# Optimization experiments

Hardware: AMD Instinct MI355X
Metric: run time of the kernel (lower is better)

## Reference

```python
import jax, jax.numpy as jnp
import numpy as np

B, T, D = 4, 1024, 1024
H = 16
DH = D // H            # head dim (attention_dim/num_heads)
FF = 4096
EPS = 1e-6             # allennlp LayerNorm eps
NEG = jnp.finfo(jnp.float32).min


def _layer_norm(x, g, b):
    # allennlp LayerNorm: (x - mean) / (unbiased_std + eps) * gamma + beta
    mean = jnp.mean(x, axis=-1, keepdims=True)
    var = jnp.var(x, axis=-1, keepdims=True) * (x.shape[-1] / (x.shape[-1] - 1))
    return g * (x - mean) / (jnp.sqrt(var) + EPS) + b


def setup_inputs() -> dict:
    key = jax.random.key(0)
    ks = jax.random.split(key, 12)
    s = lambda fan_in: 1.0 / np.sqrt(fan_in)
    return {
        "src": jax.random.normal(ks[0], (B, T, D), jnp.float32),
        "src_mask": jnp.ones((B, T), jnp.int32),
        # weights stored [in, out]
        "q_w": jax.random.uniform(ks[1], (D, D), jnp.float32, -s(D), s(D)),
        "q_b": jnp.zeros((D,), jnp.float32),
        "kv_w": jax.random.uniform(ks[2], (D, 2 * D), jnp.float32, -s(D), s(D)),
        "kv_b": jnp.zeros((2 * D,), jnp.float32),
        "out_w": jax.random.uniform(ks[3], (D, D), jnp.float32, -s(D), s(D)),
        "out_b": jnp.zeros((D,), jnp.float32),
        "ffn_w1": jax.random.uniform(ks[4], (D, FF), jnp.float32, -s(D), s(D)),
        "ffn_b1": jnp.zeros((FF,), jnp.float32),
        "ffn_w2": jax.random.uniform(ks[5], (FF, D), jnp.float32, -s(FF), s(FF)),
        "ffn_b2": jnp.zeros((D,), jnp.float32),
        "norm1_g": jnp.ones((D,), jnp.float32),
        "norm1_b": jnp.zeros((D,), jnp.float32),
        "norm2_g": jnp.ones((D,), jnp.float32),
        "norm2_b": jnp.zeros((D,), jnp.float32),
    }


def reference(src, src_mask, q_w, q_b, kv_w, kv_b, out_w, out_b,
              ffn_w1, ffn_b1, ffn_w2, ffn_b2,
              norm1_g, norm1_b, norm2_g, norm2_b):
    b, t, d = src.shape
    scale = jnp.asarray(DH ** 0.5, src.dtype)

    q = (src @ q_w + q_b).reshape(b, t, H, DH)
    kv = src @ kv_w + kv_b                         # (b,t,2D): first half keys, second half values
    k = kv[..., :D].reshape(b, t, H, DH)
    v = kv[..., D:].reshape(b, t, H, DH)

    # scaled dot-product: queries divided by sqrt(head_dim) before bmm
    logits = jnp.einsum("bqhd,bkhd->bhqk", q / scale, k)
    # memory_efficient masked_softmax: masked key positions -> dtype min
    mask = src_mask[:, None, None, :].astype(bool)  # (b,1,1,t) over keys
    logits = jnp.where(mask, logits, NEG)
    attn = jax.nn.softmax(logits, axis=-1)          # dropout off (eval)

    ctx = jnp.einsum("bhqk,bkhd->bqhd", attn, v).reshape(b, t, D)
    attn_out = ctx @ out_w + out_b

    out1 = _layer_norm(src + attn_out, norm1_g, norm1_b)
    ffn = jax.nn.relu(out1 @ ffn_w1 + ffn_b1) @ ffn_w2 + ffn_b2
    out2 = _layer_norm(out1 + ffn, norm2_g, norm2_b)
    return out2
```

## Files before the change

kernel.cpp:

```cpp
#include <hip/hip_runtime.h>

#define DEV __device__ __forceinline__
#define SB0 __builtin_amdgcn_sched_barrier(0)

typedef unsigned short u16;
typedef __attribute__((ext_vector_type(4))) float f32x4;
typedef __attribute__((ext_vector_type(8))) short short8;

DEV u16 f2bf(float f) {
  union { float f; unsigned u; } c; c.f = f;
  unsigned u = c.u;
  unsigned r = (u + 0x7FFFu + ((u >> 16) & 1u)) >> 16;
  return (u16)r;
}
DEV float bf2f(u16 h) {
  union { unsigned u; float f; } c; c.u = ((unsigned)h) << 16;
  return c.f;
}
DEV unsigned cvtpk(float a, float b) {
  unsigned r;
  asm("v_cvt_pk_bf16_f32 %0, %1, %2" : "=v"(r) : "v"(a), "v"(b));
  return r;
}

DEV void gload16(const void* g, void* l) {
  __builtin_amdgcn_global_load_lds(
      (__attribute__((address_space(1))) void*)(g),
      (__attribute__((address_space(3))) void*)(l), 16, 0, 0);
}
DEV void vmc8() { asm volatile("s_waitcnt vmcnt(8)" ::: "memory"); SB0; }
DEV void vmc0() { asm volatile("s_waitcnt vmcnt(0)" ::: "memory"); SB0; }

__global__ __launch_bounds__(256) void prep_kernel(
    const float* __restrict__ src, const float* __restrict__ q_w,
    const float* __restrict__ kv_w, const float* __restrict__ out_w,
    const float* __restrict__ w1, const float* __restrict__ w2,
    u16* __restrict__ Xbf, u16* __restrict__ WqkvT, u16* __restrict__ WoT,
    u16* __restrict__ W1T, u16* __restrict__ W2T) {
  __shared__ float tile[32 * 33];
  int bb = blockIdx.x, tid = threadIdx.x;
  if (bb < 4096) {
    int i = bb * 256 + tid;
    float4 v = reinterpret_cast<const float4*>(src)[i];
    ushort4 o;
    o.x = f2bf(v.x); o.y = f2bf(v.y); o.z = f2bf(v.z); o.w = f2bf(v.w);
    reinterpret_cast<ushort4*>(Xbf)[i] = o;
    return;
  }
  const float* in; u16* outp; int ld_in, ld_out, bx, by;
  if (bb < 5120)       { int t = bb - 4096;  in = q_w;   outp = WqkvT; ld_in = 1024; ld_out = 1024; bx = t & 31;  by = t >> 5; }
  else if (bb < 7168)  { int t = bb - 5120;  in = kv_w;  outp = WqkvT + (size_t)1024 * 1024; ld_in = 2048; ld_out = 1024; bx = t & 63;  by = t >> 6; }
  else if (bb < 8192)  { int t = bb - 7168;  in = out_w; outp = WoT;   ld_in = 1024; ld_out = 1024; bx = t & 31;  by = t >> 5; }
  else if (bb < 12288) { int t = bb - 8192;  in = w1;    outp = W1T;   ld_in = 4096; ld_out = 1024; bx = t & 127; by = t >> 7; }
  else                 { int t = bb - 12288; in = w2;    outp = W2T;   ld_in = 1024; ld_out = 4096; bx = t & 31;  by = t >> 5; }
  int tx = tid & 31, ty = tid >> 5;
  int c0 = bx * 32, r0 = by * 32;
#pragma unroll
  for (int j = 0; j < 4; ++j)
    tile[(ty + j * 8) * 33 + tx] = in[(size_t)(r0 + ty + j * 8) * ld_in + c0 + tx];
  __syncthreads();
#pragma unroll
  for (int j = 0; j < 4; ++j)
    outp[(size_t)(c0 + ty + j * 8) * ld_out + r0 + tx] = f2bf(tile[tx * 33 + ty + j * 8]);
}

__global__ __launch_bounds__(256) void transpose_vtp_kernel(
    const u16* __restrict__ in, u16* __restrict__ out) {
  __shared__ float tile[32][33];
  int c0 = blockIdx.x * 32, r0 = blockIdx.y * 32;
  int tx = threadIdx.x, ty = threadIdx.y;
#pragma unroll
  for (int j = 0; j < 4; ++j)
    tile[ty + j * 8][tx] = bf2f(in[(size_t)(r0 + ty + j * 8) * 3072 + 2048 + c0 + tx]);
  __syncthreads();
  int k = r0 + tx;
  int base = k & ~63, kb = k & 63;
  int n = kb >> 4, w = kb & 15;
  int p = ((n >> 1) << 5) | ((w >> 2) << 3) | ((n & 1) << 2) | (w & 3);
#pragma unroll
  for (int j = 0; j < 4; ++j)
    out[(size_t)(c0 + ty + j * 8) * 4096 + base + p] = f2bf(tile[tx][ty + j * 8]);
}

template <int BM, int NWARP, typename OutT, bool RELU>
__global__ __launch_bounds__(NWARP * 64, 2) void gemm_ring_kernel(
    const u16* __restrict__ A, int lda,
    const u16* __restrict__ Bt, int ldb,
    const float* __restrict__ bias, const float* __restrict__ bias2, int split,
    OutT* __restrict__ C, int ldc, int K, float scale) {
  constexpr int MT = BM / 32;
  constexpr int PWR = BM / 2;
  constexpr int WN = NWARP / 2;
  constexpr int SLOT = 2 * BM * 32;
  __shared__ __align__(16) u16 ring[4][SLOT];

  const int tid = threadIdx.x;
  const int lane = tid & 63, wid = tid >> 6;
  const int wr = wid / WN, wc = wid % WN;
  const int lr = lane & 15, hi = lane >> 4;

  const int gx = gridDim.x;
  const int nwg = gx * gridDim.y;
  const int orig = blockIdx.y * gx + blockIdx.x;
  const int q = nwg >> 3, r8 = nwg & 7, xcd = orig & 7, oo = orig >> 3;
  const int lid = (xcd < r8 ? xcd * (q + 1) : r8 * (q + 1) + (xcd - r8) * q) + oo;
  const int rb = lid / gx, cb = lid % gx;

  const u16* Abase = A + (size_t)rb * BM * lda;
  const u16* Bbase = Bt + (size_t)cb * BM * ldb;

  auto stage = [&](int slot, int kt) {
#pragma unroll
    for (int j = 0; j < 2; ++j) {
      int ch = wid * 2 + j;
      int row = ch * 16 + (lane >> 2);
      int cs = (lane & 3) ^ ((row >> 1) & 3);
      gload16(Abase + (size_t)row * lda + kt * 32 + cs * 8, &ring[slot][ch * 512]);
      gload16(Bbase + (size_t)row * ldb + kt * 32 + cs * 8, &ring[slot][BM * 32 + ch * 512]);
    }
  };

  f32x4 acc[MT][4];
  const f32x4 zero = {0.f, 0.f, 0.f, 0.f};
#pragma unroll
  for (int m = 0; m < MT; ++m)
#pragma unroll
    for (int n = 0; n < 4; ++n) acc[m][n] = zero;

  const int NT = K >> 5;
  stage(0, 0); stage(1, 1); stage(2, 2);
  vmc8();
  __builtin_amdgcn_s_barrier(); SB0;

  const int sw = (lr >> 1) & 3;
  for (int k = 0; k < NT; ++k) {
    const u16* la = &ring[k & 3][0];
    const u16* lb = &ring[k & 3][BM * 32];
    short8 bf[4], af[MT];
#pragma unroll
    for (int n = 0; n < 4; ++n)
      bf[n] = *(const short8*)(lb + (wc * 64 + n * 16 + lr) * 32 + ((hi ^ sw) * 8));
#pragma unroll
    for (int m = 0; m < MT; ++m)
      af[m] = *(const short8*)(la + (wr * PWR + m * 16 + lr) * 32 + ((hi ^ sw) * 8));
    if (k + 3 < NT) stage((k + 3) & 3, k + 3);
    __builtin_amdgcn_s_setprio(1);
#pragma unroll
    for (int m = 0; m < MT; ++m)
#pragma unroll
      for (int n = 0; n < 4; ++n)
        acc[m][n] = __builtin_amdgcn_mfma_f32_16x16x32_bf16(af[m], bf[n], acc[m][n], 0, 0, 0);
    __builtin_amdgcn_s_setprio(0);
    if (k + 4 < NT) vmc8();
    else if (k + 1 < NT) vmc0();
    __builtin_amdgcn_s_barrier(); SB0;
  }

#pragma unroll
  for (int m = 0; m < MT; ++m) {
    int row0 = rb * BM + wr * PWR + m * 16 + hi * 4;
#pragma unroll
    for (int n = 0; n < 4; ++n) {
      int col = cb * BM + wc * 64 + n * 16 + lr;
      float bv = 0.0f, sc = scale;
      if (col < split) bv = bias[col];
      else { bv = bias2[col - split]; sc = 1.0f; }
#pragma unroll
      for (int r = 0; r < 4; ++r) {
        float v = (acc[m][n][r] + bv) * sc;
        if (RELU) v = fmaxf(v, 0.0f);
        if constexpr (sizeof(OutT) == 2)
          C[(size_t)(row0 + r) * ldc + col] = f2bf(v);
        else
          C[(size_t)(row0 + r) * ldc + col] = v;
      }
    }
  }
}

__global__ __launch_bounds__(512, 2) void attn_kernel(
    const u16* __restrict__ QKV, const u16* __restrict__ Vtp,
    const int* __restrict__ mask, u16* __restrict__ CTX) {
  __shared__ __align__(16) u16 kl[2][64 * 64];
  __shared__ __align__(16) u16 vl[2][64 * 64];
  __shared__ unsigned long long mask_lds[16];
  const int lane = threadIdx.x & 63;
  const int wid = threadIdx.x >> 6;
  const int lr = lane & 15, hi = lane >> 4;
  const int bh = blockIdx.x, qt = blockIdx.y;
  const int b = bh >> 4, h = bh & 15;

  const size_t qrow = (size_t)(b * 1024 + qt * 128 + wid * 16 + lr);
  short8 qf[2];
#pragma unroll
  for (int ks = 0; ks < 2; ++ks)
    qf[ks] = *(const short8*)(QKV + qrow * 3072 + h * 64 + ks * 32 + hi * 8);

#pragma unroll
  for (int i = 0; i < 2; ++i) {
    int kt = wid * 2 + i;
    unsigned long long bal = __ballot(mask[b * 1024 + kt * 64 + lane] != 0);
    if (lane == 0) mask_lds[kt] = bal;
  }

  const u16* Kbase = QKV + (size_t)(b * 1024) * 3072 + 1024 + h * 64;
  const u16* Vbase = Vtp + (size_t)(h * 64) * 4096 + b * 1024;

  auto stage = [&](int bf, int kt) {
    int r = wid * 8 + (lane >> 3);
    int cs = (lane & 7) ^ (r & 7);
    gload16(Kbase + (size_t)(kt * 64 + r) * 3072 + cs * 8, &kl[bf][wid * 8 * 64]);
    gload16(Vbase + (size_t)r * 4096 + kt * 64 + cs * 8, &vl[bf][wid * 8 * 64]);
  };

  float m_run = -3.0e38f, l_run = 0.0f;
  f32x4 O[4];
  const f32x4 zero = {0.f, 0.f, 0.f, 0.f};
#pragma unroll
  for (int d = 0; d < 4; ++d) O[d] = zero;

  stage(0, 0);
  __syncthreads();
  int cur = 0;
  for (int kt = 0; kt < 16; ++kt) {
    if (kt + 1 < 16) stage(cur ^ 1, kt + 1);

    f32x4 s[4];
#pragma unroll
    for (int n = 0; n < 4; ++n) s[n] = zero;
    __builtin_amdgcn_s_setprio(1);
#pragma unroll
    for (int n = 0; n < 4; ++n) {
      int key = n * 16 + lr;
#pragma unroll
      for (int ks = 0; ks < 2; ++ks) {
        int ch = (hi + 4 * ks) ^ (key & 7);
        short8 kf = *(const short8*)(kl[cur] + key * 64 + ch * 8);
        s[n] = __builtin_amdgcn_mfma_f32_16x16x32_bf16(kf, qf[ks], s[n], 0, 0, 0);
      }
    }
    __builtin_amdgcn_s_setprio(0);

    unsigned long long mk = mask_lds[kt];
    if (mk != ~0ull) {
#pragma unroll
      for (int n = 0; n < 4; ++n)
#pragma unroll
        for (int r = 0; r < 4; ++r)
          if (!((mk >> (n * 16 + hi * 4 + r)) & 1ull)) s[n][r] = -3.0e38f;
    }

    float tm = -3.0e38f;
#pragma unroll
    for (int n = 0; n < 4; ++n)
      tm = fmaxf(tm, fmaxf(fmaxf(s[n][0], s[n][1]), fmaxf(s[n][2], s[n][3])));
    tm = fmaxf(tm, __shfl_xor(tm, 16));
    tm = fmaxf(tm, __shfl_xor(tm, 32));

    float mo = m_run;
    bool grow = __any(tm > mo);
    float mn = grow ? fmaxf(mo, tm) : mo;
    m_run = mn;
    float ps = 0.0f;
#pragma unroll
    for (int n = 0; n < 4; ++n)
#pragma unroll
      for (int r = 0; r < 4; ++r) {
        float p = __expf(s[n][r] - mn);
        s[n][r] = p;
        ps += p;
      }
    if (grow) {
      float alpha = __expf(mo - mn);
      l_run = l_run * alpha + ps;
#pragma unroll
      for (int d = 0; d < 4; ++d)
#pragma unroll
        for (int r = 0; r < 4; ++r) O[d][r] *= alpha;
    } else {
      l_run += ps;
    }

#pragma unroll
    for (int ks = 0; ks < 2; ++ks) {
      union { unsigned u[4]; short8 s8; } pf;
      pf.u[0] = cvtpk(s[2 * ks][0], s[2 * ks][1]);
      pf.u[1] = cvtpk(s[2 * ks][2], s[2 * ks][3]);
      pf.u[2] = cvtpk(s[2 * ks + 1][0], s[2 * ks + 1][1]);
      pf.u[3] = cvtpk(s[2 * ks + 1][2], s[2 * ks + 1][3]);
      __builtin_amdgcn_s_setprio(1);
#pragma unroll
      for (int d = 0; d < 4; ++d) {
        int vrow = d * 16 + lr;
        int ch = (hi + 4 * ks) ^ (vrow & 7);
        short8 vf = *(const short8*)(vl[cur] + vrow * 64 + ch * 8);
        O[d] = __builtin_amdgcn_mfma_f32_16x16x32_bf16(vf, pf.s8, O[d], 0, 0, 0);
      }
      __builtin_amdgcn_s_setprio(0);
    }
    __syncthreads();
    cur ^= 1;
  }

  float l = l_run;
  l += __shfl_xor(l, 16);
  l += __shfl_xor(l, 32);
  float inv = 1.0f / l;
#pragma unroll
  for (int dt = 0; dt < 4; ++dt) {
    uint2 w;
    w.x = cvtpk(O[dt][0] * inv, O[dt][1] * inv);
    w.y = cvtpk(O[dt][2] * inv, O[dt][3] * inv);
    *(uint2*)(CTX + qrow * 1024 + h * 64 + dt * 16 + hi * 4) = w;
  }
}

__global__ __launch_bounds__(256) void ln_kernel(
    const float* __restrict__ xa, const float* __restrict__ xb,
    const float* __restrict__ xc,
    const float* __restrict__ g, const float* __restrict__ beta,
    float* __restrict__ of, u16* __restrict__ ob) {
  int row = blockIdx.x;
  int tid = threadIdx.x;
  const float* pa = xa + (size_t)row * 1024;
  const float* pb = xb + (size_t)row * 1024;
  const float* pc = xc ? xc + (size_t)row * 1024 : nullptr;
  float v[4];
  float s = 0.f, s2 = 0.f;
#pragma unroll
  for (int j = 0; j < 4; ++j) {
    int c = tid + j * 256;
    float x = pa[c] + pb[c];
    if (pc) x += pc[c];
    v[j] = x; s += x; s2 += x * x;
  }
#pragma unroll
  for (int d = 1; d < 64; d <<= 1) {
    s += __shfl_xor(s, d);
    s2 += __shfl_xor(s2, d);
  }
  __shared__ float red[8];
  int w = tid >> 6, lane = tid & 63;
  if (lane == 0) { red[w] = s; red[4 + w] = s2; }
  __syncthreads();
  s = red[0] + red[1] + red[2] + red[3];
  s2 = red[4] + red[5] + red[6] + red[7];
  float mean = s * (1.0f / 1024.0f);
  float var = fmaxf((s2 - 1024.0f * mean * mean) * (1.0f / 1023.0f), 0.0f);
  float rden = 1.0f / (sqrtf(var) + 1e-6f);
#pragma unroll
  for (int j = 0; j < 4; ++j) {
    int c = tid + j * 256;
    float y = g[c] * (v[j] - mean) * rden + beta[c];
    of[(size_t)row * 1024 + c] = y;
    if (ob) ob[(size_t)row * 1024 + c] = f2bf(y);
  }
}

extern "C" void kernel_launch(void* const* d_in, const int* in_sizes, int n_in,
                              void* d_out, int out_size, void* d_ws, size_t ws_size,
                              hipStream_t stream) {
  const float* src   = (const float*)d_in[0];
  const int*   mask  = (const int*)d_in[1];
  const float* q_w   = (const float*)d_in[2];
  const float* q_b   = (const float*)d_in[3];
  const float* kv_w  = (const float*)d_in[4];
  const float* kv_b  = (const float*)d_in[5];
  const float* out_w = (const float*)d_in[6];
  const float* out_b = (const float*)d_in[7];
  const float* w1    = (const float*)d_in[8];
  const float* b1    = (const float*)d_in[9];
  const float* w2    = (const float*)d_in[10];
  const float* b2    = (const float*)d_in[11];
  const float* g1    = (const float*)d_in[12];
  const float* be1   = (const float*)d_in[13];
  const float* g2    = (const float*)d_in[14];
  const float* be2   = (const float*)d_in[15];
  float* out = (float*)d_out;

  char* ws = (char*)d_ws;
  const size_t MB = 1024 * 1024;
  const int BIG = 1 << 30;
  u16*  Xbf   = (u16*)(ws + 0);
  u16*  CTX   = (u16*)(ws + 8 * MB);
  u16*  WqkvT = (u16*)(ws + 16 * MB);
  u16*  WoT   = (u16*)(ws + 22 * MB);
  u16*  W1T   = (u16*)(ws + 24 * MB);
  u16*  W2T   = (u16*)(ws + 32 * MB);
  u16*  QKV   = (u16*)(ws + 40 * MB);
  u16*  Vtp   = (u16*)(ws + 64 * MB);
  u16*  F1b   = (u16*)(ws + 40 * MB);
  float* AOUT = (float*)(ws + 72 * MB);
  float* OUT1F= (float*)(ws + 88 * MB);
  u16*  OUT1B = (u16*)(ws + 104 * MB);
  float* F2F  = (float*)(ws + 72 * MB);

  prep_kernel<<<dim3(16384), dim3(256), 0, stream>>>(
      src, q_w, kv_w, out_w, w1, w2, Xbf, WqkvT, WoT, W1T, W2T);
  gemm_ring_kernel<256, 8, u16, false><<<dim3(12, 16), dim3(512), 0, stream>>>(
      Xbf, 1024, WqkvT, 1024, q_b, kv_b, 1024, QKV, 3072, 1024, 0.125f);
  transpose_vtp_kernel<<<dim3(32, 128), dim3(32, 8), 0, stream>>>(QKV, Vtp);
  attn_kernel<<<dim3(64, 8), dim3(512), 0, stream>>>(QKV, Vtp, mask, CTX);
  gemm_ring_kernel<128, 4, float, false><<<dim3(8, 32), dim3(256), 0, stream>>>(
      CTX, 1024, WoT, 1024, out_b, nullptr, BIG, AOUT, 1024, 1024, 1.0f);
  ln_kernel<<<dim3(4096), dim3(256), 0, stream>>>(src, AOUT, nullptr, g1, be1, OUT1F, OUT1B);
  gemm_ring_kernel<256, 8, u16, true><<<dim3(16, 16), dim3(512), 0, stream>>>(
      OUT1B, 1024, W1T, 1024, b1, nullptr, BIG, F1b, 4096, 1024, 1.0f);
  gemm_ring_kernel<128, 4, float, false><<<dim3(8, 32), dim3(256), 0, stream>>>(
      F1b, 4096, W2T, 4096, b2, nullptr, BIG, F2F, 1024, 4096, 1.0f);
  ln_kernel<<<dim3(4096), dim3(256), 0, stream>>>(OUT1F, F2F, nullptr, g2, be2, out, nullptr);
  (void)in_sizes; (void)n_in; (void)out_size; (void)ws_size;
}
```

Baseline: 316.6 us.

## Generalize GEMM tiles, use 3-slot ring, and split-K the FFN down projection

The GEMM template now takes separate BM/BN, warp grid, and occupancy parameters. The LDS ring shrinks from 4 to 3 slots with a prefetch distance of 2, which lowers LDS use so more workgroups fit per CU. The QKV, out-proj and FFN1 GEMMs use rectangular tiles that launch more blocks. The FFN2 GEMM is split-K into two partial fp32 outputs, and the second layernorm sums them with its existing third input. The trade-off is less prefetch depth, extra partial-sum traffic, and smaller tiles with less reuse.

Result: slower. 345.3 us (+9.1%).

```diff
diff --git a/kernel.cpp b/kernel.cpp
--- a/kernel.cpp
+++ b/kernel.cpp
@@ -28,8 +28,13 @@
       (__attribute__((address_space(1))) void*)(g),
       (__attribute__((address_space(3))) void*)(l), 16, 0, 0);
 }
-DEV void vmc8() { asm volatile("s_waitcnt vmcnt(8)" ::: "memory"); SB0; }
-DEV void vmc0() { asm volatile("s_waitcnt vmcnt(0)" ::: "memory"); SB0; }
+template <int N> DEV void vmcw() {
+  if constexpr (N == 0) asm volatile("s_waitcnt vmcnt(0)" ::: "memory");
+  else if constexpr (N == 3) asm volatile("s_waitcnt vmcnt(3)" ::: "memory");
+  else if constexpr (N == 4) asm volatile("s_waitcnt vmcnt(4)" ::: "memory");
+  else if constexpr (N == 8) asm volatile("s_waitcnt vmcnt(8)" ::: "memory");
+  SB0;
+}
 
 __global__ __launch_bounds__(256) void prep_kernel(
     const float* __restrict__ src, const float* __restrict__ q_w,
@@ -82,22 +87,24 @@
     out[(size_t)(c0 + ty + j * 8) * 4096 + base + p] = f2bf(tile[tx][ty + j * 8]);
 }
 
-template <int BM, int NWARP, typename OutT, bool RELU>
-__global__ __launch_bounds__(NWARP * 64, 2) void gemm_ring_kernel(
+template <int BM, int BN, int WM, int WN, int OCC, typename OutT, bool RELU>
+__global__ __launch_bounds__(WM * WN * 64, OCC) void gemm_ring_kernel(
     const u16* __restrict__ A, int lda,
     const u16* __restrict__ Bt, int ldb,
     const float* __restrict__ bias, const float* __restrict__ bias2, int split,
-    OutT* __restrict__ C, int ldc, int K, float scale) {
-  constexpr int MT = BM / 32;
-  constexpr int PWR = BM / 2;
-  constexpr int WN = NWARP / 2;
-  constexpr int SLOT = 2 * BM * 32;
-  __shared__ __align__(16) u16 ring[4][SLOT];
+    OutT* __restrict__ C, int ldc, size_t c_off, int K, float scale) {
+  constexpr int NWAVE = WM * WN;
+  constexpr int MT = BM / WM / 16;
+  constexpr int NF = BN / WN / 16;
+  constexpr int LPT = (BM + BN) / 16 / NWAVE;
+  constexpr int SLOT = (BM + BN) * 32;
+  __shared__ __align__(16) u16 ring[3][SLOT];
 
   const int tid = threadIdx.x;
   const int lane = tid & 63, wid = tid >> 6;
   const int wr = wid / WN, wc = wid % WN;
   const int lr = lane & 15, hi = lane >> 4;
+  const int z = blockIdx.z;
 
   const int gx = gridDim.x;
   const int nwg = gx * gridDim.y;
@@ -106,65 +113,71 @@
   const int lid = (xcd < r8 ? xcd * (q + 1) : r8 * (q + 1) + (xcd - r8) * q) + oo;
   const int rb = lid / gx, cb = lid % gx;
 
-  const u16* Abase = A + (size_t)rb * BM * lda;
-  const u16* Bbase = Bt + (size_t)cb * BM * ldb;
+  const u16* Abase = A + (size_t)rb * BM * lda + (size_t)z * K;
+  const u16* Bbase = Bt + (size_t)cb * BN * ldb + (size_t)z * K;
+  C += (size_t)z * c_off;
 
   auto stage = [&](int slot, int kt) {
 #pragma unroll
-    for (int j = 0; j < 2; ++j) {
-      int ch = wid * 2 + j;
-      int row = ch * 16 + (lane >> 2);
-      int cs = (lane & 3) ^ ((row >> 1) & 3);
-      gload16(Abase + (size_t)row * lda + kt * 32 + cs * 8, &ring[slot][ch * 512]);
-      gload16(Bbase + (size_t)row * ldb + kt * 32 + cs * 8, &ring[slot][BM * 32 + ch * 512]);
+    for (int j = 0; j < LPT; ++j) {
+      int u = wid * LPT + j;
+      int rloc = u * 16 + (lane >> 2);
+      int cs = (lane & 3) ^ ((rloc >> 1) & 3);
+      const u16* src;
+      if (u < BM / 16) src = Abase + (size_t)rloc * lda + kt * 32 + cs * 8;
+      else src = Bbase + (size_t)(rloc - BM) * ldb + kt * 32 + cs * 8;
+      gload16(src, &ring[slot][u * 512]);
     }
   };
 
-  f32x4 acc[MT][4];
+  f32x4 acc[MT][NF];
   const f32x4 zero = {0.f, 0.f, 0.f, 0.f};
 #pragma unroll
   for (int m = 0; m < MT; ++m)
 #pragma unroll
-    for (int n = 0; n < 4; ++n) acc[m][n] = zero;
+    for (int n = 0; n < NF; ++n) acc[m][n] = zero;
 
   const int NT = K >> 5;
-  stage(0, 0); stage(1, 1); stage(2, 2);
-  vmc8();
+  stage(0, 0); stage(1, 1);
+  vmcw<LPT>();
   __builtin_amdgcn_s_barrier(); SB0;
 
   const int sw = (lr >> 1) & 3;
+  int sl = 0, st = 2;
   for (int k = 0; k < NT; ++k) {
-    const u16* la = &ring[k & 3][0];
-    const u16* lb = &ring[k & 3][BM * 32];
-    short8 bf[4], af[MT];
-#pragma unroll
-    for (int n = 0; n < 4; ++n)
-      bf[n] = *(const short8*)(lb + (wc * 64 + n * 16 + lr) * 32 + ((hi ^ sw) * 8));
+    const u16* la = &ring[sl][0];
+    const u16* lb = &ring[sl][BM * 32];
+    short8 bf[NF], af[MT];
+#pragma unroll
+    for (int n = 0; n < NF; ++n)
+      bf[n] = *(const short8*)(lb + (wc * (BN / WN) + n * 16 + lr) * 32 + ((hi ^ sw) * 8));
 #pragma unroll
     for (int m = 0; m < MT; ++m)
-      af[m] = *(const short8*)(la + (wr * PWR + m * 16 + lr) * 32 + ((hi ^ sw) * 8));
-    if (k + 3 < NT) stage((k + 3) & 3, k + 3);
+      af[m] = *(const short8*)(la + (wr * (BM / WM) + m * 16 + lr) * 32 + ((hi ^ sw) * 8));
+    if (k + 2 < NT) stage(st, k + 2);
     __builtin_amdgcn_s_setprio(1);
 #pragma unroll
     for (int m = 0; m < MT; ++m)
 #pragma unroll
-      for (int n = 0; n < 4; ++n)
+      for (int n = 0; n < NF; ++n)
         acc[m][n] = __builtin_amdgcn_mfma_f32_16x16x32_bf16(af[m], bf[n], acc[m][n], 0, 0, 0);
     __builtin_amdgcn_s_setprio(0);
-    if (k + 4 < NT) vmc8();
-    else if (k + 1 < NT) vmc0();
+    if (k + 2 < NT) vmcw<LPT>();
+    else if (k + 1 < NT) vmcw<0>();
     __builtin_amdgcn_s_barrier(); SB0;
+    sl = (sl == 2) ? 0 : sl + 1;
+    st = (st == 2) ? 0 : st + 1;
   }
 
 #pragma unroll
   for (int m = 0; m < MT; ++m) {
-    int row0 = rb * BM + wr * PWR + m * 16 + hi * 4;
-#pragma unroll
-    for (int n = 0; n < 4; ++n) {
-      int col = cb * BM + wc * 64 + n * 16 + lr;
-      float bv = 0.0f, sc = scale;
-      if (col < split) bv = bias[col];
-      else { bv = bias2[col - split]; sc = 1.0f; }
+    int row0 = rb * BM + wr * (BM / WM) + m * 16 + hi * 4;
+#pragma unroll
+    for (int n = 0; n < NF; ++n) {
+      int col = cb * BN + wc * (BN / WN) + n * 16 + lr;
+      float sc = (col < split) ? scale : 1.0f;
+      float bv = 0.0f;
+      if (z == 0) bv = (col < split) ? bias[col] : bias2[col - split];
 #pragma unroll
       for (int r = 0; r < 4; ++r) {
         float v = (acc[m][n][r] + bv) * sc;
@@ -391,23 +404,25 @@
   u16*  Vtp   = (u16*)(ws + 64 * MB);
   u16*  F1b   = (u16*)(ws + 40 * MB);
   float* AOUT = (float*)(ws + 72 * MB);
-  float* OUT1F= (float*)(ws + 88 * MB);
-  u16*  OUT1B = (u16*)(ws + 104 * MB);
-  float* F2F  = (float*)(ws + 72 * MB);
+  float* FP0  = (float*)(ws + 72 * MB);
+  float* FP1  = (float*)(ws + 88 * MB);
+  float* OUT1F= (float*)(ws + 104 * MB);
+  u16*  OUT1B = (u16*)(ws + 0);
 
   prep_kernel<<<dim3(16384), dim3(256), 0, stream>>>(
       src, q_w, kv_w, out_w, w1, w2, Xbf, WqkvT, WoT, W1T, W2T);
-  gemm_ring_kernel<256, 8, u16, false><<<dim3(12, 16), dim3(512), 0, stream>>>(
-      Xbf, 1024, WqkvT, 1024, q_b, kv_b, 1024, QKV, 3072, 1024, 0.125f);
+  gemm_ring_kernel<256, 128, 4, 2, 4, u16, false><<<dim3(24, 16), dim3(512), 0, stream>>>(
+      Xbf, 1024, WqkvT, 1024, q_b, kv_b, 1024, QKV, 3072, 0, 1024, 0.125f);
   transpose_vtp_kernel<<<dim3(32, 128), dim3(32, 8), 0, stream>>>(QKV, Vtp);
   attn_kernel<<<dim3(64, 8), dim3(512), 0, stream>>>(QKV, Vtp, mask, CTX);
-  gemm_ring_kernel<128, 4, float, false><<<dim3(8, 32), dim3(256), 0, stream>>>(
-      CTX, 1024, WoT, 1024, out_b, nullptr, BIG, AOUT, 1024, 1024, 1.0f);
+  gemm_ring_kernel<128, 64, 2, 2, 3, float, false><<<dim3(16, 32), dim3(256), 0, stream>>>(
+      CTX, 1024, WoT, 1024, out_b, nullptr, BIG, AOUT, 1024, 0, 1024, 1.0f);
   ln_kernel<<<dim3(4096), dim3(256), 0, stream>>>(src, AOUT, nullptr, g1, be1, OUT1F, OUT1B);
-  gemm_ring_kernel<256, 8, u16, true><<<dim3(16, 16), dim3(512), 0, stream>>>(
-      OUT1B, 1024, W1T, 1024, b1, nullptr, BIG, F1b, 4096, 1024, 1.0f);
-  gemm_ring_kernel<128, 4, float, false><<<dim3(8, 32), dim3(256), 0, stream>>>(
-      F1b, 4096, W2T, 4096, b2, nullptr, BIG, F2F, 1024, 4096, 1.0f);
-  ln_kernel<<<dim3(4096), dim3(256), 0, stream>>>(OUT1F, F2F, nullptr, g2, be2, out, nullptr);
+  gemm_ring_kernel<256, 128, 4, 2, 4, u16, true><<<dim3(32, 16), dim3(512), 0, stream>>>(
+      OUT1B, 1024, W1T, 1024, b1, nullptr, BIG, F1b, 4096, 0, 1024, 1.0f);
+  gemm_ring_kernel<128, 128, 2, 2, 3, float, false><<<dim3(8, 32, 2), dim3(256), 0, stream>>>(
+      F1b, 4096, W2T, 4096, b2, nullptr, BIG, FP0, 1024,
+      (size_t)(FP1 - FP0), 2048, 1.0f);
+  ln_kernel<<<dim3(4096), dim3(256), 0, stream>>>(OUT1F, FP0, FP1, g2, be2, out, nullptr);
   (void)in_sizes; (void)n_in; (void)out_size; (void)ws_size;
 }
```
